# Kernel optimization log

Hardware: AMD Instinct MI355X
Metric: run time of the kernel (lower is better)

Reference implementation:

```python
import jax, jax.numpy as jnp
import numpy as np

EPS = 1e-6
N_SRC = 100000
N_TAR = 100000
N = N_SRC + N_TAR
DIM = 128
E = 600000
NEG_SLOPE = 0.01  # torch leaky_relu default


def setup_inputs() -> dict:
    key = jax.random.key(0)
    ks = jax.random.split(key, 8)
    x_src = jax.random.normal(ks[0], (N_SRC, DIM), dtype=jnp.float32)
    x_tar = jax.random.normal(ks[1], (N_TAR, DIM), dtype=jnp.float32)
    edge_index = jax.random.randint(ks[2], (2, E), 0, N, dtype=jnp.int64)
    edge_weight = jax.random.uniform(ks[3], (E,), dtype=jnp.float32)
    W_gcn = jax.random.normal(ks[4], (DIM, DIM), dtype=jnp.float32) / np.sqrt(DIM)
    b_gcn = jax.random.normal(ks[5], (DIM,), dtype=jnp.float32) * 0.01
    W_fnn = jax.random.normal(ks[6], (DIM, DIM), dtype=jnp.float32) / np.sqrt(DIM)
    b_fnn = jax.random.normal(ks[7], (DIM,), dtype=jnp.float32) * 0.01
    return dict(x_src=x_src, x_tar=x_tar, edge_index=edge_index,
                edge_weight=edge_weight, W_gcn=W_gcn, b_gcn=b_gcn,
                W_fnn=W_fnn, b_fnn=b_fnn)


def _gcn_conv(x, edge_index, edge_weight, W, b):
    # PyG GCNConv with add_self_loops=True, symmetric normalization.
    row = jnp.concatenate([edge_index[0], jnp.arange(N, dtype=edge_index.dtype)])
    col = jnp.concatenate([edge_index[1], jnp.arange(N, dtype=edge_index.dtype)])
    w = jnp.concatenate([edge_weight, jnp.ones((N,), dtype=edge_weight.dtype)])
    deg = jax.ops.segment_sum(w, col, num_segments=N)
    dinv = jnp.where(deg > 0, jax.lax.rsqrt(deg), 0.0)
    norm = dinv[row] * w * dinv[col]                 # [E+N]
    h = x @ W                                        # [N, D]
    msg = norm[:, None] * h[row]                     # gather + scale
    out = jnp.zeros_like(h).at[col].add(msg)         # scatter-add to targets
    return out + b


def _node_norm(x):
    mean = jnp.mean(x, axis=1, keepdims=True)
    var = jnp.mean((x - mean) ** 2, axis=1, keepdims=True)  # unbiased=False
    return (x - mean) / jnp.sqrt(var + EPS)


def reference(x_src, x_tar, edge_index, edge_weight, W_gcn, b_gcn, W_fnn, b_fnn):
    x = jnp.concatenate([x_src, x_tar], axis=0)      # [N, D]
    # route == 'MIX': GNN branch + FNN branch on the skip copy
    g = _gcn_conv(x, edge_index, edge_weight, W_gcn, b_gcn)
    f = jax.nn.leaky_relu(x @ W_fnn + b_fnn, NEG_SLOPE)  # dropout = identity (eval)
    x = g + f
    x = _node_norm(x)
    x = jax.nn.leaky_relu(x, NEG_SLOPE)
    return x[:N_SRC, :], x[N_SRC:, :]
```

## Files before the change

### kernel.cpp

```cpp
#include <hip/hip_runtime.h>
#include <hip/hip_bf16.h>
#include <cstddef>
#include <cstdint>

#define DIM 128
#define SCAN_CHUNK 2048

typedef __attribute__((ext_vector_type(8))) short short8v;
typedef __attribute__((ext_vector_type(4))) float f32x4;

__device__ __forceinline__ float leaky(float v) {
    return v > 0.0f ? v : 0.01f * v;
}

__device__ __forceinline__ unsigned short f2bf(float f) {
    unsigned u = __builtin_bit_cast(unsigned, f);
    u += 0x7FFF + ((u >> 16) & 1);
    return (unsigned short)(u >> 16);
}

__device__ __forceinline__ unsigned cvt_pk_bf16(float a, float b) {
    unsigned r;
    asm("v_cvt_pk_bf16_f32 %0, %1, %2" : "=v"(r) : "v"(a), "v"(b));
    return r;
}

__device__ __forceinline__ float bf2f_hi(unsigned p) {
    return __builtin_bit_cast(float, p & 0xFFFF0000u);
}
__device__ __forceinline__ float bf2f_lo(unsigned p) {
    return __builtin_bit_cast(float, p << 16);
}

__device__ __forceinline__ void gload_lds16(const float* g, float* lds) {
    __builtin_amdgcn_global_load_lds(
        (const __attribute__((address_space(1))) unsigned int*)g,
        (__attribute__((address_space(3))) unsigned int*)lds, 16, 0, 0);
}

__global__ __launch_bounds__(256)
void init_kernel(const float* __restrict__ Wg, const float* __restrict__ Wf,
                 unsigned short* __restrict__ WgT, unsigned short* __restrict__ WfT,
                 int* __restrict__ cnt, int N) {
    int t = blockIdx.x * 256 + threadIdx.x;
    if (t < N) cnt[t] = 0;
    if (t < 128 * 128) {
        int col = t >> 7, k = t & 127;
        WgT[col * 128 + k] = f2bf(Wg[k * 128 + col]);
        WfT[col * 128 + k] = f2bf(Wf[k * 128 + col]);
    }
}

__global__ __launch_bounds__(256)
void hist_kernel(const int* __restrict__ col, int* __restrict__ cnt, int E) {
    int e = blockIdx.x * blockDim.x + threadIdx.x;
    if (e < E) atomicAdd(&cnt[col[e]], 1);
}

__global__ __launch_bounds__(256)
void scan_block_sums(const int* __restrict__ cnt, int* __restrict__ bsum, int N) {
    __shared__ int sdata[4];
    int base = blockIdx.x * SCAN_CHUNK;
    int s = 0;
    for (int k = threadIdx.x; k < SCAN_CHUNK; k += 256) {
        int idx = base + k;
        s += (idx < N) ? cnt[idx] : 0;
    }
#pragma unroll
    for (int m = 1; m < 64; m <<= 1) s += __shfl_xor(s, m, 64);
    if ((threadIdx.x & 63) == 0) sdata[threadIdx.x >> 6] = s;
    __syncthreads();
    if (threadIdx.x == 0)
        bsum[blockIdx.x] = sdata[0] + sdata[1] + sdata[2] + sdata[3];
}

__global__ __launch_bounds__(128)
void scan_bsum_kernel(int* __restrict__ bsum, int nb) {
    __shared__ int wtot[2];
    int t = threadIdx.x;
    int lane = t & 63;
    int orig = (t < nb) ? bsum[t] : 0;
    int v = orig;
#pragma unroll
    for (int m = 1; m < 64; m <<= 1) {
        int u = __shfl_up(v, m, 64);
        if (lane >= m) v += u;
    }
    if (lane == 63) wtot[t >> 6] = v;
    __syncthreads();
    if (t >= 64) v += wtot[0];
    if (t < nb) bsum[t] = v - orig;
}

__global__ __launch_bounds__(256)
void scan_write_kernel(int* __restrict__ cnt, const int* __restrict__ bsum,
                       int* __restrict__ off, int N) {
    __shared__ int wsum[4];
    int t = threadIdx.x;
    int base = blockIdx.x * SCAN_CHUNK + t * 8;
    int vals[8];
    int local = 0;
#pragma unroll
    for (int k = 0; k < 8; ++k) {
        int idx = base + k;
        int c = (idx < N) ? cnt[idx] : 0;
        vals[k] = local;
        local += c;
    }
    int tsum = local;
    int lane = t & 63;
    int v = tsum;
#pragma unroll
    for (int m = 1; m < 64; m <<= 1) {
        int u = __shfl_up(v, m, 64);
        if (lane >= m) v += u;
    }
    if (lane == 63) wsum[t >> 6] = v;
    __syncthreads();
    int woff = 0;
    for (int i = 0; i < (t >> 6); ++i) woff += wsum[i];
    int texcl = (v - tsum) + woff + bsum[blockIdx.x];
#pragma unroll
    for (int k = 0; k < 8; ++k) {
        int idx = base + k;
        int o = texcl + vals[k];
        if (idx <= N) off[idx] = o;
    }
    __syncthreads();
#pragma unroll
    for (int k = 0; k < 8; ++k) {
        int idx = base + k;
        int o = texcl + vals[k];
        if (idx < N) cnt[idx] = o;
    }
}

__global__ __launch_bounds__(256)
void reorder_kernel(const int* __restrict__ row, const int* __restrict__ col,
                    const float* __restrict__ w, int* __restrict__ cursor,
                    int2* __restrict__ edgeRW, int E) {
    int e = blockIdx.x * blockDim.x + threadIdx.x;
    if (e < E) {
        int c = col[e];
        int pos = atomicAdd(&cursor[c], 1);
        edgeRW[pos] = make_int2(row[e], __builtin_bit_cast(int, w[e]));
    }
}

__global__ __launch_bounds__(256)
void csr_dinv_kernel(const int* __restrict__ off, const int2* __restrict__ edgeRW,
                     float* __restrict__ dinv, int N) {
    int i = blockIdx.x * 256 + threadIdx.x;
    if (i >= N) return;
    int s = off[i], e = off[i + 1];
    float acc = 1.0f;
    for (int j = s; j < e; ++j)
        acc += __builtin_bit_cast(float, edgeRW[j].y);
    dinv[i] = rsqrtf(acc);
}

__global__ __launch_bounds__(512, 4)
void gemm_mfma_kernel(const float* __restrict__ x_src, const float* __restrict__ x_tar,
                      int n_src, int n_total,
                      const unsigned short* __restrict__ WgT,
                      const unsigned short* __restrict__ WfT,
                      const float* __restrict__ bg, const float* __restrict__ bf,
                      const float* __restrict__ dinv,
                      unsigned short* __restrict__ hsb,
                      unsigned short* __restrict__ accb)
{
    __shared__ float Ash[128 * 128];

    const int t  = threadIdx.x;
    const int wv = t >> 6;

#pragma unroll
    for (int s = 0; s < 8; ++s) {
        int id  = s * 512 + t;
        int row = id >> 5;
        int cs  = id & 31;
        int c   = cs ^ (row & 15);
        int rg  = blockIdx.x * 128 + row;
        if (rg >= n_total) rg = n_total - 1;
        const float* xr = (rg < n_src) ? x_src + (size_t)rg * DIM
                                       : x_tar + (size_t)(rg - n_src) * DIM;
        gload_lds16(xr + c * 4, &Ash[(size_t)(s * 512 + wv * 64) * 4]);
    }
    __syncthreads();

    const int lane = t & 63;
    const int wr = wv >> 2;
    const int wc = wv & 3;
    const int lr = lane & 15;
    const int lk = lane >> 4;

    f32x4 accg[4][2], accf[4][2];
#pragma unroll
    for (int i = 0; i < 4; ++i)
#pragma unroll
        for (int j = 0; j < 2; ++j) {
            accg[i][j] = (f32x4)0.0f;
            accf[i][j] = (f32x4)0.0f;
        }

#pragma unroll
    for (int ks = 0; ks < 4; ++ks) {
        short8v xf[4];
#pragma unroll
        for (int mf = 0; mf < 4; ++mf) {
            int row = wr * 64 + mf * 16 + lr;
            int c0  = ks * 8 + lk * 2;
            float4 q0 = *(const float4*)&Ash[(size_t)(row * 32 + ( c0      ^ (row & 15))) * 4];
            float4 q1 = *(const float4*)&Ash[(size_t)(row * 32 + ((c0 + 1) ^ (row & 15))) * 4];
            union { short8v v; unsigned u[4]; } cv;
            cv.u[0] = cvt_pk_bf16(q0.x, q0.y);
            cv.u[1] = cvt_pk_bf16(q0.z, q0.w);
            cv.u[2] = cvt_pk_bf16(q1.x, q1.y);
            cv.u[3] = cvt_pk_bf16(q1.z, q1.w);
            xf[mf] = cv.v;
        }
#pragma unroll
        for (int nf = 0; nf < 2; ++nf) {
            int col = wc * 32 + nf * 16 + lr;
            const size_t bo = (size_t)col * 128 + ks * 32 + lk * 8;
            short8v bgv = *(const short8v*)(WgT + bo);
            short8v bfv = *(const short8v*)(WfT + bo);
#pragma unroll
            for (int mf = 0; mf < 4; ++mf) {
                accg[mf][nf] = __builtin_amdgcn_mfma_f32_16x16x32_bf16(bgv, xf[mf], accg[mf][nf], 0, 0, 0);
                accf[mf][nf] = __builtin_amdgcn_mfma_f32_16x16x32_bf16(bfv, xf[mf], accf[mf][nf], 0, 0, 0);
            }
        }
    }

#pragma unroll
    for (int mf = 0; mf < 4; ++mf) {
        int r = blockIdx.x * 128 + wr * 64 + mf * 16 + lr;
        const bool valid = (r < n_total);
        int rc = valid ? r : (n_total - 1);
        float dv = dinv[rc];
#pragma unroll
        for (int nf = 0; nf < 2; ++nf) {
            int c0 = wc * 32 + nf * 16 + lk * 4;
            float4 bgv = *(const float4*)(bg + c0);
            float4 bfv = *(const float4*)(bf + c0);

            float hs0 = dv * accg[mf][nf][0];
            float hs1 = dv * accg[mf][nf][1];
            float hs2 = dv * accg[mf][nf][2];
            float hs3 = dv * accg[mf][nf][3];

            float o0 = leaky(accf[mf][nf][0] + bfv.x) + bgv.x + dv * hs0;
            float o1 = leaky(accf[mf][nf][1] + bfv.y) + bgv.y + dv * hs1;
            float o2 = leaky(accf[mf][nf][2] + bfv.z) + bgv.z + dv * hs2;
            float o3 = leaky(accf[mf][nf][3] + bfv.w) + bgv.w + dv * hs3;

            uint2 hp, op;
            hp.x = cvt_pk_bf16(hs0, hs1);
            hp.y = cvt_pk_bf16(hs2, hs3);
            op.x = cvt_pk_bf16(o0, o1);
            op.y = cvt_pk_bf16(o2, o3);

            if (valid) {
                *(uint2*)(hsb  + (size_t)r * DIM + c0) = hp;
                *(uint2*)(accb + (size_t)r * DIM + c0) = op;
            }
        }
    }
}

__global__ __launch_bounds__(256)
void gather_norm_kernel(const int* __restrict__ off, const int2* __restrict__ edgeRW,
                        const float* __restrict__ dinv,
                        const unsigned short* __restrict__ hsb,
                        const unsigned short* __restrict__ accb,
                        float* __restrict__ out, int n)
{
    const int wid  = threadIdx.x >> 6;
    const int lane = threadIdx.x & 63;
    const int sub  = lane >> 4;
    const int sl   = lane & 15;
    int i = (blockIdx.x * 4 + wid) * 4 + sub;
    if (i >= n) i = n - 1;

    const int start = off[i];
    const int degc  = off[i + 1] - start;

    int md = degc;
    md = max(md, __shfl_xor(md, 16, 64));
    md = max(md, __shfl_xor(md, 32, 64));

    float s[8];
#pragma unroll
    for (int k = 0; k < 8; ++k) s[k] = 0.0f;

    const unsigned short* gbase = hsb + (size_t)sl * 8;

    int   r0 = 0, r1 = 0;
    float w0 = 0.0f, w1 = 0.0f;
    if (0 < degc) { int2 m = edgeRW[start];     r0 = m.x; w0 = __builtin_bit_cast(float, m.y); }
    if (1 < degc) { int2 m = edgeRW[start + 1]; r1 = m.x; w1 = __builtin_bit_cast(float, m.y); }
    uint4 p0 = *(const uint4*)(gbase + (size_t)r0 * DIM);

    for (int t = 0; t < md; ++t) {
        uint4 p1 = p0;
        if (t + 1 < md)
            p1 = *(const uint4*)(gbase + (size_t)r1 * DIM);
        int r2 = 0; float w2 = 0.0f;
        if (t + 2 < md) {
            if (t + 2 < degc) {
                int2 m = edgeRW[start + t + 2];
                r2 = m.x; w2 = __builtin_bit_cast(float, m.y);
            }
        }
        s[0] += w0 * bf2f_lo(p0.x); s[1] += w0 * bf2f_hi(p0.x);
        s[2] += w0 * bf2f_lo(p0.y); s[3] += w0 * bf2f_hi(p0.y);
        s[4] += w0 * bf2f_lo(p0.z); s[5] += w0 * bf2f_hi(p0.z);
        s[6] += w0 * bf2f_lo(p0.w); s[7] += w0 * bf2f_hi(p0.w);
        p0 = p1;
        r0 = r1; w0 = w1;
        r1 = r2; w1 = w2;
    }

    const float dv = dinv[i];
    uint4 av = *(const uint4*)(accb + (size_t)i * DIM + sl * 8);
    float v[8];
    v[0] = bf2f_lo(av.x) + dv * s[0]; v[1] = bf2f_hi(av.x) + dv * s[1];
    v[2] = bf2f_lo(av.y) + dv * s[2]; v[3] = bf2f_hi(av.y) + dv * s[3];
    v[4] = bf2f_lo(av.z) + dv * s[4]; v[5] = bf2f_hi(av.z) + dv * s[5];
    v[6] = bf2f_lo(av.w) + dv * s[6]; v[7] = bf2f_hi(av.w) + dv * s[7];

    float sum = 0.0f;
#pragma unroll
    for (int k = 0; k < 8; ++k) sum += v[k];
#pragma unroll
    for (int m = 1; m < 16; m <<= 1) sum += __shfl_xor(sum, m, 64);
    const float mean = sum * (1.0f / 128.0f);

    float sq = 0.0f;
#pragma unroll
    for (int k = 0; k < 8; ++k) {
        v[k] -= mean;
        sq += v[k] * v[k];
    }
#pragma unroll
    for (int m = 1; m < 16; m <<= 1) sq += __shfl_xor(sq, m, 64);
    const float rstd = rsqrtf(sq * (1.0f / 128.0f) + 1e-6f);

    float4 o1, o2;
    o1.x = leaky(v[0] * rstd); o1.y = leaky(v[1] * rstd);
    o1.z = leaky(v[2] * rstd); o1.w = leaky(v[3] * rstd);
    o2.x = leaky(v[4] * rstd); o2.y = leaky(v[5] * rstd);
    o2.z = leaky(v[6] * rstd); o2.w = leaky(v[7] * rstd);
    float* op = out + (size_t)i * DIM + sl * 8;
    *(float4*)op       = o1;
    *(float4*)(op + 4) = o2;
}

extern "C" void kernel_launch(void* const* d_in, const int* in_sizes, int n_in,
                              void* d_out, int out_size, void* d_ws, size_t ws_size,
                              hipStream_t stream)
{
    const float* x_src = (const float*)d_in[0];
    const float* x_tar = (const float*)d_in[1];
    const int*   ei    = (const int*)d_in[2];
    const float* ew    = (const float*)d_in[3];
    const float* Wg    = (const float*)d_in[4];
    const float* bg    = (const float*)d_in[5];
    const float* Wf    = (const float*)d_in[6];
    const float* bf    = (const float*)d_in[7];

    const int n_src = in_sizes[0] / DIM;
    const int n_tar = in_sizes[1] / DIM;
    const int N     = n_src + n_tar;
    const int E     = in_sizes[3];

    const int* rowp = ei;
    const int* colp = ei + E;

    char* p = (char*)d_ws;
    float* dinv = (float*)p;  p += (size_t)N * 4;
    int*   cnt  = (int*)p;    p += (size_t)N * 4;
    int*   off  = (int*)p;    p += (size_t)(N + 1) * 4;
    int*   bsum = (int*)p;    p += 160 * 4;
    p = (char*)(((uintptr_t)p + 15) & ~(uintptr_t)15);
    int2*  edgeRW = (int2*)p; p += (size_t)E * 8;
    unsigned short* hsb  = (unsigned short*)p; p += (size_t)N * DIM * 2;
    unsigned short* accb = (unsigned short*)p; p += (size_t)N * DIM * 2;
    unsigned short* WgT  = (unsigned short*)p; p += 128 * 128 * 2;
    unsigned short* WfT  = (unsigned short*)p;

    const int NB = (N + 1 + SCAN_CHUNK - 1) / SCAN_CHUNK;

    init_kernel<<<(N + 255) / 256, 256, 0, stream>>>(Wg, Wf, WgT, WfT, cnt, N);

    hist_kernel<<<(E + 255) / 256, 256, 0, stream>>>(colp, cnt, E);

    scan_block_sums<<<NB, 256, 0, stream>>>(cnt, bsum, N);
    scan_bsum_kernel<<<1, 128, 0, stream>>>(bsum, NB);
    scan_write_kernel<<<NB, 256, 0, stream>>>(cnt, bsum, off, N);

    reorder_kernel<<<(E + 255) / 256, 256, 0, stream>>>(rowp, colp, ew, cnt,
                                                        edgeRW, E);

    csr_dinv_kernel<<<(N + 255) / 256, 256, 0, stream>>>(off, edgeRW, dinv, N);

    gemm_mfma_kernel<<<(N + 127) / 128, 512, 0, stream>>>(
        x_src, x_tar, n_src, N, WgT, WfT, bg, bf, dinv, hsb, accb);

    gather_norm_kernel<<<(N + 15) / 16, 256, 0, stream>>>(
        off, edgeRW, dinv, hsb, accb, (float*)d_out, N);
}
```

Baseline: 215.9 us.

## Make GEMM persistent with double-buffered LDS tiles and register-resident weights

The dense GEMM kernel becomes a persistent kernel. A fixed grid of 512 blocks strides over 64-row tiles, and each block keeps both bf16 weight fragments in registers for its whole lifetime. The next tile's activations are prefetched into a second LDS buffer while the current tile is computed, so global loads overlap MFMA work and the weights are not reloaded per tile. In exchange, each block has a smaller tile, the GPU holds fewer blocks in flight, and the kernel depends on the barrier at the top of the loop to wait for the asynchronous LDS loads.

```diff
diff --git a/kernel.cpp b/kernel.cpp
--- a/kernel.cpp
+++ b/kernel.cpp
@@ -161,7 +161,7 @@
 
 __global__ __launch_bounds__(512, 4)
 void gemm_mfma_kernel(const float* __restrict__ x_src, const float* __restrict__ x_tar,
-                      int n_src, int n_total,
+                      int n_src, int n_total, int ntiles,
                       const unsigned short* __restrict__ WgT,
                       const unsigned short* __restrict__ WfT,
                       const float* __restrict__ bg, const float* __restrict__ bf,
@@ -169,103 +169,120 @@
                       unsigned short* __restrict__ hsb,
                       unsigned short* __restrict__ accb)
 {
-    __shared__ float Ash[128 * 128];
-
-    const int t  = threadIdx.x;
-    const int wv = t >> 6;
-
-#pragma unroll
-    for (int s = 0; s < 8; ++s) {
-        int id  = s * 512 + t;
-        int row = id >> 5;
-        int cs  = id & 31;
-        int c   = cs ^ (row & 15);
-        int rg  = blockIdx.x * 128 + row;
-        if (rg >= n_total) rg = n_total - 1;
-        const float* xr = (rg < n_src) ? x_src + (size_t)rg * DIM
-                                       : x_tar + (size_t)(rg - n_src) * DIM;
-        gload_lds16(xr + c * 4, &Ash[(size_t)(s * 512 + wv * 64) * 4]);
-    }
-    __syncthreads();
-
+    __shared__ float Ash[2][64 * 128];
+
+    const int t    = threadIdx.x;
     const int lane = t & 63;
-    const int wr = wv >> 2;
-    const int wc = wv & 3;
-    const int lr = lane & 15;
-    const int lk = lane >> 4;
-
-    f32x4 accg[4][2], accf[4][2];
-#pragma unroll
-    for (int i = 0; i < 4; ++i)
-#pragma unroll
-        for (int j = 0; j < 2; ++j) {
-            accg[i][j] = (f32x4)0.0f;
-            accf[i][j] = (f32x4)0.0f;
+    const int wv   = t >> 6;
+    const int h    = wv >> 2;
+    const int q    = wv & 3;
+    const int lr   = lane & 15;
+    const int lk   = lane >> 4;
+    const int nb   = gridDim.x;
+
+    short8v wg[4][2], wf[4][2];
+#pragma unroll
+    for (int ks = 0; ks < 4; ++ks)
+#pragma unroll
+        for (int nf = 0; nf < 2; ++nf) {
+            int col = q * 32 + nf * 16 + lr;
+            const size_t bo = (size_t)col * 128 + ks * 32 + lk * 8;
+            wg[ks][nf] = *(const short8v*)(WgT + bo);
+            wf[ks][nf] = *(const short8v*)(WfT + bo);
         }
 
-#pragma unroll
-    for (int ks = 0; ks < 4; ++ks) {
-        short8v xf[4];
-#pragma unroll
-        for (int mf = 0; mf < 4; ++mf) {
-            int row = wr * 64 + mf * 16 + lr;
-            int c0  = ks * 8 + lk * 2;
-            float4 q0 = *(const float4*)&Ash[(size_t)(row * 32 + ( c0      ^ (row & 15))) * 4];
-            float4 q1 = *(const float4*)&Ash[(size_t)(row * 32 + ((c0 + 1) ^ (row & 15))) * 4];
-            union { short8v v; unsigned u[4]; } cv;
-            cv.u[0] = cvt_pk_bf16(q0.x, q0.y);
-            cv.u[1] = cvt_pk_bf16(q0.z, q0.w);
-            cv.u[2] = cvt_pk_bf16(q1.x, q1.y);
-            cv.u[3] = cvt_pk_bf16(q1.z, q1.w);
-            xf[mf] = cv.v;
+    auto stage = [&](int tl, int buf) {
+#pragma unroll
+        for (int s = 0; s < 4; ++s) {
+            int id  = s * 512 + t;
+            int row = id >> 5;
+            int cs  = id & 31;
+            int c   = cs ^ (row & 15);
+            int rg  = tl * 64 + row;
+            if (rg >= n_total) rg = n_total - 1;
+            const float* xr = (rg < n_src) ? x_src + (size_t)rg * DIM
+                                           : x_tar + (size_t)(rg - n_src) * DIM;
+            gload_lds16(xr + c * 4, &Ash[buf][(size_t)(s * 512 + wv * 64) * 4]);
         }
-#pragma unroll
-        for (int nf = 0; nf < 2; ++nf) {
-            int col = wc * 32 + nf * 16 + lr;
-            const size_t bo = (size_t)col * 128 + ks * 32 + lk * 8;
-            short8v bgv = *(const short8v*)(WgT + bo);
-            short8v bfv = *(const short8v*)(WfT + bo);
-#pragma unroll
-            for (int mf = 0; mf < 4; ++mf) {
-                accg[mf][nf] = __builtin_amdgcn_mfma_f32_16x16x32_bf16(bgv, xf[mf], accg[mf][nf], 0, 0, 0);
-                accf[mf][nf] = __builtin_amdgcn_mfma_f32_16x16x32_bf16(bfv, xf[mf], accf[mf][nf], 0, 0, 0);
+    };
+
+    int tile = blockIdx.x;
+    if (tile < ntiles) stage(tile, 0);
+    int cur = 0;
+
+    for (; tile < ntiles; tile += nb) {
+        __syncthreads();
+        if (tile + nb < ntiles) stage(tile + nb, cur ^ 1);
+
+        f32x4 accg[2][2], accf[2][2];
+#pragma unroll
+        for (int i = 0; i < 2; ++i)
+#pragma unroll
+            for (int j = 0; j < 2; ++j) {
+                accg[i][j] = (f32x4)0.0f;
+                accf[i][j] = (f32x4)0.0f;
+            }
+
+#pragma unroll
+        for (int ks = 0; ks < 4; ++ks) {
+            short8v xf[2];
+#pragma unroll
+            for (int mf = 0; mf < 2; ++mf) {
+                int row = h * 32 + mf * 16 + lr;
+                int c0  = ks * 8 + lk * 2;
+                float4 q0 = *(const float4*)&Ash[cur][(size_t)(row * 32 + ( c0      ^ (row & 15))) * 4];
+                float4 q1 = *(const float4*)&Ash[cur][(size_t)(row * 32 + ((c0 + 1) ^ (row & 15))) * 4];
+                union { short8v v; unsigned u[4]; } cv;
+                cv.u[0] = cvt_pk_bf16(q0.x, q0.y);
+                cv.u[1] = cvt_pk_bf16(q0.z, q0.w);
+                cv.u[2] = cvt_pk_bf16(q1.x, q1.y);
+                cv.u[3] = cvt_pk_bf16(q1.z, q1.w);
+                xf[mf] = cv.v;
+            }
+#pragma unroll
+            for (int nf = 0; nf < 2; ++nf)
+#pragma unroll
+                for (int mf = 0; mf < 2; ++mf) {
+                    accg[mf][nf] = __builtin_amdgcn_mfma_f32_16x16x32_bf16(wg[ks][nf], xf[mf], accg[mf][nf], 0, 0, 0);
+                    accf[mf][nf] = __builtin_amdgcn_mfma_f32_16x16x32_bf16(wf[ks][nf], xf[mf], accf[mf][nf], 0, 0, 0);
+                }
+        }
+
+#pragma unroll
+        for (int mf = 0; mf < 2; ++mf) {
+            int r = tile * 64 + h * 32 + mf * 16 + lr;
+            const bool valid = (r < n_total);
+            int rc = valid ? r : (n_total - 1);
+            float dv = dinv[rc];
+#pragma unroll
+            for (int nf = 0; nf < 2; ++nf) {
+                int c0 = q * 32 + nf * 16 + lk * 4;
+                float4 bgv = *(const float4*)(bg + c0);
+                float4 bfv = *(const float4*)(bf + c0);
+
+                float hs0 = dv * accg[mf][nf][0];
+                float hs1 = dv * accg[mf][nf][1];
+                float hs2 = dv * accg[mf][nf][2];
+                float hs3 = dv * accg[mf][nf][3];
+
+                float o0 = leaky(accf[mf][nf][0] + bfv.x) + bgv.x + dv * hs0;
+                float o1 = leaky(accf[mf][nf][1] + bfv.y) + bgv.y + dv * hs1;
+                float o2 = leaky(accf[mf][nf][2] + bfv.z) + bgv.z + dv * hs2;
+                float o3 = leaky(accf[mf][nf][3] + bfv.w) + bgv.w + dv * hs3;
+
+                uint2 hp, op;
+                hp.x = cvt_pk_bf16(hs0, hs1);
+                hp.y = cvt_pk_bf16(hs2, hs3);
+                op.x = cvt_pk_bf16(o0, o1);
+                op.y = cvt_pk_bf16(o2, o3);
+
+                if (valid) {
+                    *(uint2*)(hsb  + (size_t)r * DIM + c0) = hp;
+                    *(uint2*)(accb + (size_t)r * DIM + c0) = op;
+                }
             }
         }
-    }
-
-#pragma unroll
-    for (int mf = 0; mf < 4; ++mf) {
-        int r = blockIdx.x * 128 + wr * 64 + mf * 16 + lr;
-        const bool valid = (r < n_total);
-        int rc = valid ? r : (n_total - 1);
-        float dv = dinv[rc];
-#pragma unroll
-        for (int nf = 0; nf < 2; ++nf) {
-            int c0 = wc * 32 + nf * 16 + lk * 4;
-            float4 bgv = *(const float4*)(bg + c0);
-            float4 bfv = *(const float4*)(bf + c0);
-
-            float hs0 = dv * accg[mf][nf][0];
-            float hs1 = dv * accg[mf][nf][1];
-            float hs2 = dv * accg[mf][nf][2];
-            float hs3 = dv * accg[mf][nf][3];
-
-            float o0 = leaky(accf[mf][nf][0] + bfv.x) + bgv.x + dv * hs0;
-            float o1 = leaky(accf[mf][nf][1] + bfv.y) + bgv.y + dv * hs1;
-            float o2 = leaky(accf[mf][nf][2] + bfv.z) + bgv.z + dv * hs2;
-            float o3 = leaky(accf[mf][nf][3] + bfv.w) + bgv.w + dv * hs3;
-
-            uint2 hp, op;
-            hp.x = cvt_pk_bf16(hs0, hs1);
-            hp.y = cvt_pk_bf16(hs2, hs3);
-            op.x = cvt_pk_bf16(o0, o1);
-            op.y = cvt_pk_bf16(o2, o3);
-
-            if (valid) {
-                *(uint2*)(hsb  + (size_t)r * DIM + c0) = hp;
-                *(uint2*)(accb + (size_t)r * DIM + c0) = op;
-            }
-        }
+        cur ^= 1;
     }
 }
 
@@ -405,8 +422,9 @@
 
     csr_dinv_kernel<<<(N + 255) / 256, 256, 0, stream>>>(off, edgeRW, dinv, N);
 
-    gemm_mfma_kernel<<<(N + 127) / 128, 512, 0, stream>>>(
-        x_src, x_tar, n_src, N, WgT, WfT, bg, bf, dinv, hsb, accb);
+    const int ntiles = (N + 63) / 64;
+    gemm_mfma_kernel<<<512, 512, 0, stream>>>(
+        x_src, x_tar, n_src, N, ntiles, WgT, WfT, bg, bf, dinv, hsb, accb);
 
     gather_norm_kernel<<<(N + 15) / 16, 256, 0, stream>>>(
         off, edgeRW, dinv, hsb, accb, (float*)d_out, N);
```

Result: slower. 226.2 us (+4.8%).
